# Kernel optimization log

Measured on AMD Instinct MI355X. Metric: run time of the kernel, lower is better.

Reference implementation:

```python
import jax, jax.numpy as jnp
import numpy as np

EPS = 1e-06


def setup_inputs() -> dict:
    key = jax.random.key(0)
    k1, k2 = jax.random.split(key)
    L, B, N, T = 5, 16, 4096, 96
    # intervals with start < end (sort last dim), like real proposals/targets
    reg_pred = jnp.sort(jax.random.uniform(k1, (L, B, N, 2), dtype=jnp.float32), axis=-1)
    reg_gt = jnp.sort(jax.random.uniform(k2, (L, B, T, 2), dtype=jnp.float32), axis=-1)
    return {"reg_pred": reg_pred, "reg_gt": reg_gt, "batch_size": B}


def _safe_div(num, den, cond):
    # avoid NaN/inf from masked-out lanes
    return jnp.where(cond, num / jnp.where(cond, den, 1.0), 0.0)


def reference(reg_pred, reg_gt, batch_size):
    # reg_pred: [L,B,N,2] anchors (start,end); reg_gt: [L,B,T,2] targets
    s = reg_pred[..., :, None, 0]  # [L,B,N,1]
    e = reg_pred[..., :, None, 1]  # [L,B,N,1]
    a = reg_gt[..., None, :, 0]    # [L,B,1,T]
    b = reg_gt[..., None, :, 1]    # [L,B,1,T]

    c0 = (s < a) & (e > b)
    c1 = (s < a) & (e < b) & (e > a)
    c2 = (s > a) & (s < b) & (e > b)

    iou = (_safe_div(b - a, e - s, c0)
           + _safe_div(e - a, b - s, c1)
           + _safe_div(b - s, e - a, c2))
    iou = jnp.where(iou < EPS, 1.0, iou)

    # loss per (layer, batch, target) = sum over anchors of -log(iou)
    loss_lbt = -jnp.sum(jnp.log(iou), axis=2)  # [L,B,T]
    # original resets the loss list each layer -> only last layer survives
    return jnp.sum(loss_lbt[-1]) / batch_size
```

## Files before the change

### kernel.cpp

```cpp
#include <hip/hip_runtime.h>

#define EPS 1e-6f
#define NBLK 1024

__global__ __launch_bounds__(256) void iou_partial_kernel(
    const float2* __restrict__ pred4,
    const float2* __restrict__ gt4,
    float* __restrict__ partial)
{
    __shared__ float2 gts[24];
    __shared__ float wave_part[4];

    const int tid = threadIdx.x;
    const int blk = blockIdx.x;
    const int b  = blk >> 6;
    const int nc = (blk >> 2) & 15;
    const int tc = blk & 3;

    if (tid < 24) gts[tid] = gt4[b * 96 + tc * 24 + tid];
    __syncthreads();

    const float2 p = pred4[b * 4096 + nc * 256 + tid];
    const float s = p.x, e = p.y;

    float acc = 0.0f;
#pragma unroll
    for (int t = 0; t < 24; ++t) {
        const float a  = gts[t].x;
        const float bb = gts[t].y;
        const bool c0 = (s < a) & (e > bb);
        const bool c1 = (s < a) & (e < bb) & (e > a);
        const bool c2 = (s > a) & (s < bb) & (e > bb);
        const float num = c0 ? (bb - a) : (c1 ? (e - a) : (bb - s));
        const float den = c0 ? (e - s)  : (c1 ? (bb - s) : (e - a));
        const bool valid = (c0 | c1 | c2) && (num >= EPS * den);
        const float contrib = __log2f(num) - __log2f(den);
        acc += valid ? contrib : 0.0f;
    }

    for (int off = 32; off; off >>= 1)
        acc += __shfl_down(acc, off);
    if ((tid & 63) == 0) wave_part[tid >> 6] = acc;
    __syncthreads();
    if (tid == 0)
        partial[blk] = wave_part[0] + wave_part[1] + wave_part[2] + wave_part[3];
}

__global__ __launch_bounds__(256) void iou_final_kernel(
    const float* __restrict__ partial,
    const int* __restrict__ bs_ptr,
    float* __restrict__ out)
{
    __shared__ float wave_part[4];
    const int tid = threadIdx.x;

    float v = 0.0f;
#pragma unroll
    for (int i = 0; i < NBLK / 256; ++i)
        v += partial[i * 256 + tid];

    for (int off = 32; off; off >>= 1)
        v += __shfl_down(v, off);
    if ((tid & 63) == 0) wave_part[tid >> 6] = v;
    __syncthreads();

    if (tid == 0) {
        const float total = wave_part[0] + wave_part[1] + wave_part[2] + wave_part[3];
        out[0] = total * (-0.69314718055994531f / (float)bs_ptr[0]);
    }
}

extern "C" void kernel_launch(void* const* d_in, const int* in_sizes, int n_in,
                              void* d_out, int out_size, void* d_ws, size_t ws_size,
                              hipStream_t stream) {
    (void)in_sizes; (void)n_in; (void)ws_size; (void)out_size;

    const float* pred = (const float*)d_in[0];
    const float* gt   = (const float*)d_in[1];
    const int*   bs   = (const int*)d_in[2];
    float*       out  = (float*)d_out;
    float*       partial = (float*)d_ws;

    const int L = 5, B = 16, N = 4096, T = 96;
    const float2* pred4 = (const float2*)pred + (size_t)(L - 1) * B * N;
    const float2* gt4   = (const float2*)gt   + (size_t)(L - 1) * B * T;

    iou_partial_kernel<<<dim3(NBLK), dim3(256), 0, stream>>>(pred4, gt4, partial);
    iou_final_kernel<<<dim3(1), dim3(256), 0, stream>>>(partial, bs, out);
}
```

Before: 14.37 us.

## Fuse partial and final reduction into one cooperative kernel with grid sync

Replaces the two-kernel reduction with a single cooperative launch of 256 blocks. Each block now handles all 96 targets for its 256 anchors instead of splitting targets four ways, and block 0 does the final sum after a grid-wide sync. This removes the second kernel launch and its launch gap. In exchange there are fewer blocks with longer loops, plus the cost of a grid barrier and cooperative launch overhead.

```diff
diff --git a/kernel.cpp b/kernel.cpp
--- a/kernel.cpp
+++ b/kernel.cpp
@@ -1,31 +1,34 @@
 #include <hip/hip_runtime.h>
+#include <hip/hip_cooperative_groups.h>
+
+namespace cg = cooperative_groups;
 
 #define EPS 1e-6f
-#define NBLK 1024
 
-__global__ __launch_bounds__(256) void iou_partial_kernel(
+__global__ __launch_bounds__(256) void iou_coop_kernel(
     const float2* __restrict__ pred4,
     const float2* __restrict__ gt4,
+    const int* __restrict__ bs_ptr,
+    float* __restrict__ out,
     float* __restrict__ partial)
 {
-    __shared__ float2 gts[24];
+    __shared__ float2 gts[96];
     __shared__ float wave_part[4];
 
     const int tid = threadIdx.x;
     const int blk = blockIdx.x;
-    const int b  = blk >> 6;
-    const int nc = (blk >> 2) & 15;
-    const int tc = blk & 3;
+    const int b  = blk >> 4;
+    const int nc = blk & 15;
 
-    if (tid < 24) gts[tid] = gt4[b * 96 + tc * 24 + tid];
+    if (tid < 96) gts[tid] = gt4[b * 96 + tid];
     __syncthreads();
 
     const float2 p = pred4[b * 4096 + nc * 256 + tid];
     const float s = p.x, e = p.y;
 
     float acc = 0.0f;
-#pragma unroll
-    for (int t = 0; t < 24; ++t) {
+#pragma unroll 8
+    for (int t = 0; t < 96; ++t) {
         const float a  = gts[t].x;
         const float bb = gts[t].y;
         const bool c0 = (s < a) & (e > bb);
@@ -44,29 +47,19 @@
     __syncthreads();
     if (tid == 0)
         partial[blk] = wave_part[0] + wave_part[1] + wave_part[2] + wave_part[3];
-}
 
-__global__ __launch_bounds__(256) void iou_final_kernel(
-    const float* __restrict__ partial,
-    const int* __restrict__ bs_ptr,
-    float* __restrict__ out)
-{
-    __shared__ float wave_part[4];
-    const int tid = threadIdx.x;
+    cg::this_grid().sync();
 
-    float v = 0.0f;
-#pragma unroll
-    for (int i = 0; i < NBLK / 256; ++i)
-        v += partial[i * 256 + tid];
-
-    for (int off = 32; off; off >>= 1)
-        v += __shfl_down(v, off);
-    if ((tid & 63) == 0) wave_part[tid >> 6] = v;
-    __syncthreads();
-
-    if (tid == 0) {
-        const float total = wave_part[0] + wave_part[1] + wave_part[2] + wave_part[3];
-        out[0] = total * (-0.69314718055994531f / (float)bs_ptr[0]);
+    if (blk == 0) {
+        float v = partial[tid];
+        for (int off = 32; off; off >>= 1)
+            v += __shfl_down(v, off);
+        if ((tid & 63) == 0) wave_part[tid >> 6] = v;
+        __syncthreads();
+        if (tid == 0) {
+            const float total = wave_part[0] + wave_part[1] + wave_part[2] + wave_part[3];
+            out[0] = total * (-0.69314718055994531f / (float)bs_ptr[0]);
+        }
     }
 }
 
@@ -85,6 +78,7 @@
     const float2* pred4 = (const float2*)pred + (size_t)(L - 1) * B * N;
     const float2* gt4   = (const float2*)gt   + (size_t)(L - 1) * B * T;
 
-    iou_partial_kernel<<<dim3(NBLK), dim3(256), 0, stream>>>(pred4, gt4, partial);
-    iou_final_kernel<<<dim3(1), dim3(256), 0, stream>>>(partial, bs, out);
+    void* args[] = {(void*)&pred4, (void*)&gt4, (void*)&bs, (void*)&out, (void*)&partial};
+    hipLaunchCooperativeKernel((const void*)iou_coop_kernel,
+                               dim3(B * 16), dim3(256), args, 0, stream);
 }
```

Measured after the change: 52.54 us. 266% more time.
